# Kernel tuning notes

Measured on AMD Instinct MI355X. Metric: run time of the kernel, lower is better.

## Reference

```python
import jax, jax.numpy as jnp
import numpy as np

VOCAB, DIM, LAYERS = 32000, 1024, 4
B, L = 8, 512


def setup_inputs() -> dict:
    key = jax.random.key(0)
    ks = jax.random.split(key, 8)
    s = 0.02
    return {
        "input_ids": jax.random.randint(ks[0], (B, L), 0, VOCAB),
        "embed_W": jax.random.normal(ks[1], (VOCAB, DIM), jnp.float32) * s,
        "h_starter": jax.random.normal(ks[2], (LAYERS, DIM), jnp.float32) * s,
        "gate_W": jax.random.normal(ks[3], (LAYERS, 2 * DIM, 2 * DIM), jnp.float32) * s,
        "gate_b": jnp.zeros((LAYERS, 2 * DIM), jnp.float32),
        "cand_W": jax.random.normal(ks[4], (LAYERS, DIM, 2 * DIM), jnp.float32) * s,
        "cand_b": jnp.zeros((LAYERS, DIM), jnp.float32),
        "out_W": jax.random.normal(ks[5], (VOCAB, DIM), jnp.float32) * s,
    }


def _gru_forward(input_ids, embed_W, h_starter, gate_W, gate_b, cand_W, cand_b, out_W):
    Bsz = input_ids.shape[0]
    x = embed_W[input_ids]                      # [B, L, D]
    h0 = jnp.broadcast_to(h_starter[:, None, :], (LAYERS, Bsz, DIM))  # [Ly, B, D]

    def step(h, x_t):
        # h: [Ly, B, D], x_t: [B, D]
        new_h = []
        xin = x_t
        for i in range(LAYERS):
            hi = h[i]
            xh = jnp.concatenate([xin, hi], axis=-1)           # [B, 2D]
            g = xh @ gate_W[i].T + gate_b[i]                   # [B, 2D]
            z, r = jnp.split(g, 2, axis=-1)
            z = jax.nn.sigmoid(z)
            r = jax.nn.sigmoid(r)
            cin = jnp.concatenate([xin, r * hi], axis=-1)      # [B, 2D]
            cand = jnp.tanh(cin @ cand_W[i].T + cand_b[i])     # [B, D]
            hn = z * hi + (1.0 - z) * cand
            new_h.append(hn)
            xin = hn
        return jnp.stack(new_h), xin

    _, ys = jax.lax.scan(step, h0, jnp.swapaxes(x, 0, 1))      # ys: [L, B, D]
    ys = jnp.swapaxes(ys, 0, 1)                                # [B, L, D]
    logits = jnp.einsum('bld,vd->blv', ys, out_W)              # [B, L, V]
    return logits


def reference(input_ids, embed_W, h_starter, gate_W, gate_b, cand_W, cand_b, out_W):
    return _gru_forward(input_ids, embed_W, h_starter, gate_W, gate_b, cand_W, cand_b, out_W)
```

## Files before the change

kernel.cpp:

```cpp
#include <hip/hip_runtime.h>
#include <hip/hip_bf16.h>

#define VOCAB  32000
#define DIM    1024
#define NLAYER 4
#define NB     8
#define SEQ    512

#define NGROUP       4
#define GBLKS        64
#define SCAN_BLOCKS  (NGROUP * GBLKS)
#define SCAN_THREADS 512
#define ROWH         2056

typedef __attribute__((ext_vector_type(8))) short          bf16x8;
typedef __attribute__((ext_vector_type(4))) float          f32x4;
typedef __attribute__((ext_vector_type(2))) float          f32x2;
typedef __attribute__((ext_vector_type(8))) unsigned short u16x8;
typedef __attribute__((ext_vector_type(4))) unsigned short u16x4;
typedef __attribute__((ext_vector_type(8))) _Float16       h8f;
typedef __attribute__((ext_vector_type(4))) _Float16       h4f;

__device__ __forceinline__ u16x8 cvt8_bf16(const float* p) {
    float4 f0 = *(const float4*)p;
    float4 f1 = *(const float4*)(p + 4);
    union { __hip_bfloat16 h[8]; u16x8 v; } u;
    u.h[0] = __float2bfloat16(f0.x); u.h[1] = __float2bfloat16(f0.y);
    u.h[2] = __float2bfloat16(f0.z); u.h[3] = __float2bfloat16(f0.w);
    u.h[4] = __float2bfloat16(f1.x); u.h[5] = __float2bfloat16(f1.y);
    u.h[6] = __float2bfloat16(f1.z); u.h[7] = __float2bfloat16(f1.w);
    return u.v;
}

__device__ __forceinline__ h8f pack8(f32x4 a, f32x4 b) {
    h8f o;
    o[0] = (_Float16)a[0]; o[1] = (_Float16)a[1];
    o[2] = (_Float16)a[2]; o[3] = (_Float16)a[3];
    o[4] = (_Float16)b[0]; o[5] = (_Float16)b[1];
    o[6] = (_Float16)b[2]; o[7] = (_Float16)b[3];
    return o;
}

__device__ __forceinline__ void ld4v(f32x4& d, const float* p) {
    asm volatile("global_load_dwordx4 %0, %1, off sc0 sc1"
                 : "=&v"(d) : "v"(p));
}
__device__ __forceinline__ void st8v(void* p, f32x2 v) {
    asm volatile("global_store_dwordx2 %0, %1, off sc0 sc1"
                 :: "v"(p), "v"(v) : "memory");
}
__device__ __forceinline__ void st2v(void* p, unsigned v) {
    asm volatile("global_store_short %0, %1, off sc0 sc1"
                 :: "v"(p), "v"(v) : "memory");
}
__device__ __forceinline__ void vmwait0() {
    asm volatile("s_waitcnt vmcnt(0)" ::: "memory");
}

__global__ void bar_init_kernel(unsigned* __restrict__ bar) {
    bar[threadIdx.x]        = 0u;
    bar[threadIdx.x + 1024] = 0u;
    bar[threadIdx.x + 2048] = 0u;
    bar[threadIdx.x + 3072] = 0u;
}

__device__ __forceinline__ void slot_bar(unsigned* __restrict__ slots, int bkg,
                                         unsigned seq, bool& dead) {
    __syncthreads();
    const int tid = threadIdx.x;
    if (tid == 0)
        __hip_atomic_store(&slots[bkg * 8], seq, __ATOMIC_RELAXED,
                           __HIP_MEMORY_SCOPE_AGENT);
    if (tid < 64 && !dead) {
        unsigned guard = 0;
        for (;;) {
            unsigned v = __hip_atomic_load(&slots[tid * 8], __ATOMIC_RELAXED,
                                           __HIP_MEMORY_SCOPE_AGENT);
            if (__all((int)(v >= seq))) break;
            __builtin_amdgcn_s_sleep(1);
            if (++guard > (1u << 16)) { dead = true; break; }
        }
    }
    __syncthreads();
}

__global__ void __launch_bounds__(SCAN_THREADS)
__attribute__((amdgpu_waves_per_eu(2, 2)))
gru_scan(
    const int*   __restrict__ ids,
    const float* __restrict__ embW,
    const float* __restrict__ hstart,
    const float* __restrict__ gW,
    const float* __restrict__ gB,
    const float* __restrict__ cW,
    const float* __restrict__ cB,
    _Float16* __restrict__ hbuf16,
    _Float16* __restrict__ rbuf16,
    __hip_bfloat16* __restrict__ ysfb,
    unsigned* __restrict__ bar,
    const float* __restrict__ outW,
    __hip_bfloat16* __restrict__ outWb,
    int doConv)
{
    __shared__ _Float16 act[NB][ROWH];
    __shared__ float pz[4][4][64];
    __shared__ float pr[4][4][64];
    __shared__ float pc[2][4][64];
    __shared__ float pcb[2][4][64];
    __shared__ float hb[4][64];

    const int tid   = threadIdx.x;
    const int lane  = tid & 63;
    const int wv    = tid >> 6;
    const int l15   = lane & 15;
    const int lgq   = lane >> 4;
    const int bcol  = l15 & 7;
    const int g     = blockIdx.x >> 6;
    const int bkg   = blockIdx.x & (GBLKS-1);
    const int jbase = bkg * 16;
    const int jrow  = jbase + l15;

    if (doConv && g > 0) {
        const int cidx = (blockIdx.x - GBLKS) * SCAN_THREADS + tid;
        for (int u = cidx; u < VOCAB * DIM / 8; u += (SCAN_BLOCKS - GBLKS) * SCAN_THREADS)
            ((u16x8*)outWb)[u] = cvt8_bf16(outW + (size_t)u * 8);
    }

    h8f Wa[16], Wb[16];
    if (wv < 6) {
        const float* wzp = gW + ((size_t)g * 2048 + jrow) * 2048;
        const float* wrp = gW + ((size_t)g * 2048 + 1024 + jrow) * 2048;
        const float* wcp = cW + ((size_t)g * 1024 + jrow) * 2048;
        const float* baseA; const float* baseB; int koA, koB;
        switch (wv) {
          case 0:  baseA = wzp; koA = 0;    baseB = wrp; koB = 0;    break;
          case 1:  baseA = wzp; koA = 512;  baseB = wrp; koB = 512;  break;
          case 2:  baseA = wzp; koA = 1024; baseB = wrp; koB = 1024; break;
          case 3:  baseA = wzp; koA = 1536; baseB = wrp; koB = 1536; break;
          case 4:  baseA = wcp; koA = 0;    baseB = wcp; koB = 1024; break;
          default: baseA = wcp; koA = 512;  baseB = wcp; koB = 1536; break;
        }
        #pragma unroll
        for (int kc = 0; kc < 16; ++kc) {
            const int ka = koA + kc * 32 + lgq * 8;
            const int kb = koB + kc * 32 + lgq * 8;
            Wa[kc] = pack8(*(const f32x4*)(baseA + ka), *(const f32x4*)(baseA + ka + 4));
            Wb[kc] = pack8(*(const f32x4*)(baseB + kb), *(const f32x4*)(baseB + kb + 4));
        }
        #pragma unroll
        for (int kc = 0; kc < 16; ++kc) {
            asm volatile("" : "+v"(Wa[kc]));
            asm volatile("" : "+v"(Wb[kc]));
        }
    }

    float bz4[4], br4[4], cb4[4], hold[4], zreg[4];
    if (wv == 6) {
        #pragma unroll
        for (int r = 0; r < 4; ++r) {
            const int j = jbase + lgq * 4 + r;
            bz4[r]  = gB[g * 2048 + j];
            cb4[r]  = cB[g * 1024 + j];
            hold[r] = hstart[g * 1024 + j];
            hb[r][lane] = hold[r];
        }
    }
    if (wv == 7) {
        #pragma unroll
        for (int r = 0; r < 4; ++r)
            br4[r] = gB[g * 2048 + 1024 + jbase + lgq * 4 + r];
    }

    bool dead = false;
    unsigned* slots1g = bar + g * 512;
    unsigned* slots2g = bar + 2048 + g * 512;
    unsigned* s2prev  = (g > 0)          ? bar + 2048 + (g - 1) * 512 : nullptr;
    unsigned* s1next  = (g < NGROUP - 1) ? bar + (g + 1) * 512        : nullptr;
    _Float16* rbufg16 = rbuf16 + (size_t)g * NB * DIM;

    if (tid < 128) {
        int e = bkg * 128 + tid;
        union { _Float16 h; unsigned short u; } cv;
        cv.h = (_Float16)hstart[g * DIM + (e & (DIM - 1))];
        st2v(&hbuf16[((size_t)3 * NLAYER + g) * NB * DIM + e], (unsigned)cv.u);
    }
    slot_bar(slots2g, bkg, 1u, dead);

    for (int t = 0; t < SEQ; ++t) {
        const int so = (t + 3) & 3;
        const int sw = t & 3;
        const _Float16* hsrc16  = hbuf16 + ((size_t)so * NLAYER + g) * NB * DIM;
        _Float16*       hdst16  = hbuf16 + ((size_t)sw * NLAYER + g) * NB * DIM;
        const _Float16* xprev16 = hbuf16 + ((size_t)sw * NLAYER + (g > 0 ? g - 1 : 0)) * NB * DIM;

        {
            const unsigned need_a = (g > 0) ? (unsigned)(t + 2) : 0u;
            const unsigned need_b = (g < NGROUP - 1 && t >= 4) ? (unsigned)(t - 3) : 0u;
            if (tid < 64 && !dead && (need_a | need_b)) {
                unsigned guard = 0;
                for (;;) {
                    bool ok = true;
                    if (need_a)
                        ok &= (__hip_atomic_load(&s2prev[tid * 8], __ATOMIC_RELAXED,
                                                 __HIP_MEMORY_SCOPE_AGENT) >= need_a);
                    if (need_b)
                        ok &= (__hip_atomic_load(&s1next[tid * 8], __ATOMIC_RELAXED,
                                                 __HIP_MEMORY_SCOPE_AGENT) >= need_b);
                    if (__all((int)ok)) break;
                    __builtin_amdgcn_s_sleep(1);
                    if (++guard > (1u << 16)) { dead = true; break; }
                }
            }
            __syncthreads();
        }

        if (g == 0) {
            #pragma unroll
            for (int q = 0; q < 2; ++q) {
                const int u = q * SCAN_THREADS + tid;
                const int b = u >> 7, d8 = (u & 127) * 8;
                const float* p = embW + (size_t)ids[b * SEQ + t] * DIM + d8;
                *(h8f*)&act[b][d8] = pack8(*(const f32x4*)p, *(const f32x4*)(p + 4));
            }
            f32x4 hv[2];
            #pragma unroll
            for (int q = 0; q < 2; ++q) {
                const int u = q * SCAN_THREADS + tid;
                ld4v(hv[q], (const float*)(hsrc16 + (size_t)(u >> 7) * DIM + (u & 127) * 8));
            }
            vmwait0();
            asm volatile("" : "+v"(hv[0]), "+v"(hv[1]));
            #pragma unroll
            for (int q = 0; q < 2; ++q) {
                const int u = q * SCAN_THREADS + tid;
                *(h8f*)&act[u >> 7][1024 + (u & 127) * 8] = __builtin_bit_cast(h8f, hv[q]);
            }
        } else {
            f32x4 xv[2], hv[2];
            #pragma unroll
            for (int q = 0; q < 2; ++q) {
                const int u = q * SCAN_THREADS + tid;
                ld4v(xv[q], (const float*)(xprev16 + (size_t)(u >> 7) * DIM + (u & 127) * 8));
                ld4v(hv[q], (const float*)(hsrc16 + (size_t)(u >> 7) * DIM + (u & 127) * 8));
            }
            vmwait0();
            asm volatile("" : "+v"(xv[0]), "+v"(xv[1]), "+v"(hv[0]), "+v"(hv[1]));
            #pragma unroll
            for (int q = 0; q < 2; ++q) {
                const int u = q * SCAN_THREADS + tid;
                const int b = u >> 7, d8 = (u & 127) * 8;
                *(h8f*)&act[b][d8]        = __builtin_bit_cast(h8f, xv[q]);
                *(h8f*)&act[b][1024 + d8] = __builtin_bit_cast(h8f, hv[q]);
            }
        }
        __syncthreads();

        if (wv < 6) {
            const int kb2 = (wv < 4) ? wv * 512 : (wv - 4) * 512;
            f32x4 accA = {0.f, 0.f, 0.f, 0.f};
            f32x4 accB = {0.f, 0.f, 0.f, 0.f};
            #pragma unroll
            for (int kc = 0; kc < 16; ++kc) {
                const h8f bf = *(const h8f*)&act[bcol][kb2 + kc * 32 + lgq * 8];
                accA = __builtin_amdgcn_mfma_f32_16x16x32_f16(Wa[kc], bf, accA, 0, 0, 0);
                if (wv < 4)
                    accB = __builtin_amdgcn_mfma_f32_16x16x32_f16(Wb[kc], bf, accB, 0, 0, 0);
            }
            if (wv < 4) {
                #pragma unroll
                for (int r = 0; r < 4; ++r) {
                    pz[wv][r][lane] = accA[r];
                    pr[wv][r][lane] = accB[r];
                }
            } else {
                #pragma unroll
                for (int r = 0; r < 4; ++r) pc[wv - 4][r][lane] = accA[r];
            }
        }
        __syncthreads();

        if (wv == 6) {
            #pragma unroll
            for (int r = 0; r < 4; ++r) {
                const float s = pz[0][r][lane] + pz[1][r][lane]
                              + pz[2][r][lane] + pz[3][r][lane] + bz4[r];
                zreg[r] = 1.f / (1.f + expf(-s));
            }
        }
        if (wv == 7) {
            h4f rh4;
            #pragma unroll
            for (int r = 0; r < 4; ++r) {
                const float s = pr[0][r][lane] + pr[1][r][lane]
                              + pr[2][r][lane] + pr[3][r][lane] + br4[r];
                const float rg = 1.f / (1.f + expf(-s));
                rh4[r] = (_Float16)(rg * hb[r][lane]);
            }
            if (l15 < 8)
                st8v(rbufg16 + (size_t)bcol * DIM + jbase + lgq * 4,
                     __builtin_bit_cast(f32x2, rh4));
        }
        slot_bar(slots1g, bkg, (unsigned)(t + 1), dead);

        {
            f32x4 rv[2];
            #pragma unroll
            for (int q = 0; q < 2; ++q) {
                const int u = q * SCAN_THREADS + tid;
                ld4v(rv[q], (const float*)(rbufg16 + (size_t)(u >> 7) * DIM + (u & 127) * 8));
            }
            vmwait0();
            asm volatile("" : "+v"(rv[0]), "+v"(rv[1]));
            #pragma unroll
            for (int q = 0; q < 2; ++q) {
                const int u = q * SCAN_THREADS + tid;
                *(h8f*)&act[u >> 7][(u & 127) * 8] = __builtin_bit_cast(h8f, rv[q]);
            }
        }
        __syncthreads();

        if (wv == 4 || wv == 5) {
            const int kb2 = (wv - 4) * 512;
            f32x4 acc = {0.f, 0.f, 0.f, 0.f};
            #pragma unroll
            for (int kc = 0; kc < 16; ++kc) {
                const h8f bf = *(const h8f*)&act[bcol][kb2 + kc * 32 + lgq * 8];
                acc = __builtin_amdgcn_mfma_f32_16x16x32_f16(Wb[kc], bf, acc, 0, 0, 0);
            }
            #pragma unroll
            for (int r = 0; r < 4; ++r) pcb[wv - 4][r][lane] = acc[r];
        }
        __syncthreads();

        if (wv == 6) {
            h4f hp; u16x4 yp;
            #pragma unroll
            for (int r = 0; r < 4; ++r) {
                const float cand = tanhf(pc[0][r][lane] + pc[1][r][lane]
                                         + pcb[0][r][lane] + pcb[1][r][lane] + cb4[r]);
                const float hn = zreg[r] * hold[r] + (1.f - zreg[r]) * cand;
                hold[r] = hn;
                hb[r][lane] = hn;
                hp[r] = (_Float16)hn;
                union { __hip_bfloat16 b; unsigned short u; } cv;
                cv.b = __float2bfloat16(hn);
                yp[r] = cv.u;
            }
            if (l15 < 8) {
                st8v(hdst16 + (size_t)bcol * DIM + jbase + lgq * 4,
                     __builtin_bit_cast(f32x2, hp));
                if (g == NGROUP - 1)
                    *(f32x2*)(ysfb + ((size_t)bcol * SEQ + t) * DIM + jbase + lgq * 4) =
                        __builtin_bit_cast(f32x2, yp);
            }
        }
        slot_bar(slots2g, bkg, (unsigned)(t + 2), dead);
    }

    if (dead && tid == 0) {
        union { __hip_bfloat16 b; unsigned short u; } cv;
        cv.b = __float2bfloat16(1.0e8f);
        ((unsigned short*)ysfb)[blockIdx.x] = cv.u;
    }
}

#define BM 128
#define BN 128
#define BK 64

__global__ void __launch_bounds__(256) out_gemm_bb(
    const __hip_bfloat16* __restrict__ A,
    const __hip_bfloat16* __restrict__ B,
    float* __restrict__ C)
{
    __shared__ __hip_bfloat16 At[BM][BK + 8];
    __shared__ __hip_bfloat16 Bt[BN][BK + 8];

    const int tid  = threadIdx.x;
    const int lane = tid & 63;
    const int wv   = tid >> 6;
    const int wm   = wv >> 1, wn = wv & 1;
    const int m0   = blockIdx.y * BM;
    const int n0   = blockIdx.x * BN;

    f32x4 acc[4][4];
    #pragma unroll
    for (int i = 0; i < 4; ++i)
        #pragma unroll
        for (int jj = 0; jj < 4; ++jj)
            acc[i][jj] = (f32x4){0.f, 0.f, 0.f, 0.f};

    const int srow = tid >> 3;
    const int scol = (tid & 7) * 8;
    const int l15  = lane & 15;
    const int l4   = lane >> 4;

    for (int kt = 0; kt < DIM / BK; ++kt) {
        const int k0 = kt * BK;
        #pragma unroll
        for (int rnd = 0; rnd < 4; ++rnd) {
            const int row = rnd * 32 + srow;
            *(u16x8*)&At[row][scol] =
                *(const u16x8*)&A[(size_t)(m0 + row) * DIM + k0 + scol];
            *(u16x8*)&Bt[row][scol] =
                *(const u16x8*)&B[(size_t)(n0 + row) * DIM + k0 + scol];
        }
        __syncthreads();
        #pragma unroll
        for (int ks = 0; ks < 2; ++ks) {
            bf16x8 av[4], bv[4];
            #pragma unroll
            for (int i = 0; i < 4; ++i) {
                av[i] = *(const bf16x8*)&At[wm * 64 + i * 16 + l15][ks * 32 + l4 * 8];
                bv[i] = *(const bf16x8*)&Bt[wn * 64 + i * 16 + l15][ks * 32 + l4 * 8];
            }
            #pragma unroll
            for (int i = 0; i < 4; ++i)
                #pragma unroll
                for (int jj = 0; jj < 4; ++jj)
                    acc[i][jj] = __builtin_amdgcn_mfma_f32_16x16x32_bf16(
                        av[i], bv[jj], acc[i][jj], 0, 0, 0);
        }
        __syncthreads();
    }

    const int rq = l4 * 4;
    #pragma unroll
    for (int i = 0; i < 4; ++i) {
        const int rbase = m0 + wm * 64 + i * 16 + rq;
        #pragma unroll
        for (int jj = 0; jj < 4; ++jj) {
            const int col = n0 + wn * 64 + jj * 16 + l15;
            #pragma unroll
            for (int r2 = 0; r2 < 4; ++r2)
                C[(size_t)(rbase + r2) * VOCAB + col] = acc[i][jj][r2];
        }
    }
}

__global__ void __launch_bounds__(256) out_gemm_bf(
    const __hip_bfloat16* __restrict__ A,
    const float* __restrict__ B,
    float* __restrict__ C)
{
    __shared__ __hip_bfloat16 At[BM][BK + 8];
    __shared__ __hip_bfloat16 Bt[BN][BK + 8];

    const int tid  = threadIdx.x;
    const int lane = tid & 63;
    const int wv   = tid >> 6;
    const int wm   = wv >> 1, wn = wv & 1;
    const int m0   = blockIdx.y * BM;
    const int n0   = blockIdx.x * BN;

    f32x4 acc[4][4];
    #pragma unroll
    for (int i = 0; i < 4; ++i)
        #pragma unroll
        for (int jj = 0; jj < 4; ++jj)
            acc[i][jj] = (f32x4){0.f, 0.f, 0.f, 0.f};

    const int srow = tid >> 3;
    const int scol = (tid & 7) * 8;
    const int l15  = lane & 15;
    const int l4   = lane >> 4;

    for (int kt = 0; kt < DIM / BK; ++kt) {
        const int k0 = kt * BK;
        #pragma unroll
        for (int rnd = 0; rnd < 4; ++rnd) {
            const int row = rnd * 32 + srow;
            *(u16x8*)&At[row][scol] =
                *(const u16x8*)&A[(size_t)(m0 + row) * DIM + k0 + scol];
            *(u16x8*)&Bt[row][scol] =
                cvt8_bf16(&B[(size_t)(n0 + row) * DIM + k0 + scol]);
        }
        __syncthreads();
        #pragma unroll
        for (int ks = 0; ks < 2; ++ks) {
            bf16x8 av[4], bv[4];
            #pragma unroll
            for (int i = 0; i < 4; ++i) {
                av[i] = *(const bf16x8*)&At[wm * 64 + i * 16 + l15][ks * 32 + l4 * 8];
                bv[i] = *(const bf16x8*)&Bt[wn * 64 + i * 16 + l15][ks * 32 + l4 * 8];
            }
            #pragma unroll
            for (int i = 0; i < 4; ++i)
                #pragma unroll
                for (int jj = 0; jj < 4; ++jj)
                    acc[i][jj] = __builtin_amdgcn_mfma_f32_16x16x32_bf16(
                        av[i], bv[jj], acc[i][jj], 0, 0, 0);
        }
        __syncthreads();
    }

    const int rq = l4 * 4;
    #pragma unroll
    for (int i = 0; i < 4; ++i) {
        const int rbase = m0 + wm * 64 + i * 16 + rq;
        #pragma unroll
        for (int jj = 0; jj < 4; ++jj) {
            const int col = n0 + wn * 64 + jj * 16 + l15;
            #pragma unroll
            for (int r2 = 0; r2 < 4; ++r2)
                C[(size_t)(rbase + r2) * VOCAB + col] = acc[i][jj][r2];
        }
    }
}

extern "C" void kernel_launch(void* const* d_in, const int* in_sizes, int n_in,
                              void* d_out, int out_size, void* d_ws, size_t ws_size,
                              hipStream_t stream)
{
    (void)in_sizes; (void)n_in; (void)out_size;
    const int*   ids  = (const int*)  d_in[0];
    const float* embW = (const float*)d_in[1];
    const float* hst  = (const float*)d_in[2];
    const float* gW   = (const float*)d_in[3];
    const float* gB   = (const float*)d_in[4];
    const float* cW   = (const float*)d_in[5];
    const float* cB   = (const float*)d_in[6];
    const float* outW = (const float*)d_in[7];
    float* logits = (float*)d_out;

    char* ws = (char*)d_ws;
    unsigned*       bar    = (unsigned*)ws;
    _Float16*       rbuf16 = (_Float16*)(ws + 16384);
    _Float16*       hbuf16 = (_Float16*)(ws + 16384 + 65536);
    __hip_bfloat16* ysfb   = (__hip_bfloat16*)(ws + 16384 + 65536 + 262144);
    const size_t outWb_off = 16384 + 65536 + 262144 + (size_t)NB * SEQ * DIM * 2;
    const size_t need      = outWb_off + (size_t)VOCAB * DIM * 2;
    const int doConv = (ws_size >= need) ? 1 : 0;
    __hip_bfloat16* outWb = doConv ? (__hip_bfloat16*)(ws + outWb_off) : nullptr;

    bar_init_kernel<<<dim3(1), dim3(1024), 0, stream>>>(bar);

    gru_scan<<<dim3(SCAN_BLOCKS), dim3(SCAN_THREADS), 0, stream>>>(
        ids, embW, hst, gW, gB, cW, cB, hbuf16, rbuf16, ysfb, bar,
        outW, outWb, doConv);

    if (doConv)
        out_gemm_bb<<<dim3(VOCAB / BN, (NB * SEQ) / BM), dim3(256), 0, stream>>>(
            ysfb, outWb, logits);
    else
        out_gemm_bf<<<dim3(VOCAB / BN, (NB * SEQ) / BM), dim3(256), 0, stream>>>(
            ysfb, outW, logits);
}
```

Measured before the change: 3.504 ms.

## Use direct global-to-LDS loads and XCD-aware block swizzle in output GEMM

The output projection GEMM now stages A and B tiles with global_load_lds (buffer-to-LDS DMA) instead of going through registers, and drops the LDS row padding the direct load needs. The launch grid is flattened to 1D and remapped so consecutive blocks on the same XCD share tiles, which should improve L2 reuse. Without padding the MFMA fragment reads from LDS may hit bank conflicts. The GRU scan dominates runtime, so the effect on total time is bounded.

```diff
diff --git a/kernel.cpp b/kernel.cpp
--- a/kernel.cpp
+++ b/kernel.cpp
@@ -55,6 +55,12 @@
 }
 __device__ __forceinline__ void vmwait0() {
     asm volatile("s_waitcnt vmcnt(0)" ::: "memory");
+}
+
+__device__ __forceinline__ void gload_lds16(const void* g, void* l) {
+    __builtin_amdgcn_global_load_lds(
+        (const __attribute__((address_space(1))) void*)g,
+        (__attribute__((address_space(3))) void*)l, 16, 0, 0);
 }
 
 __global__ void bar_init_kernel(unsigned* __restrict__ bar) {
@@ -373,15 +379,19 @@
     const __hip_bfloat16* __restrict__ B,
     float* __restrict__ C)
 {
-    __shared__ __hip_bfloat16 At[BM][BK + 8];
-    __shared__ __hip_bfloat16 Bt[BN][BK + 8];
+    __shared__ __hip_bfloat16 At[BM][BK];
+    __shared__ __hip_bfloat16 Bt[BN][BK];
 
     const int tid  = threadIdx.x;
     const int lane = tid & 63;
     const int wv   = tid >> 6;
     const int wm   = wv >> 1, wn = wv & 1;
-    const int m0   = blockIdx.y * BM;
-    const int n0   = blockIdx.x * BN;
+    const int l15  = lane & 15;
+    const int l4   = lane >> 4;
+
+    const int swz = (blockIdx.x & 7) * 1000 + (blockIdx.x >> 3);
+    const int n0  = (swz % 250) * BN;
+    const int m0  = (swz / 250) * BM;
 
     f32x4 acc[4][4];
     #pragma unroll
@@ -390,20 +400,18 @@
         for (int jj = 0; jj < 4; ++jj)
             acc[i][jj] = (f32x4){0.f, 0.f, 0.f, 0.f};
 
-    const int srow = tid >> 3;
+    const int srow = (tid >> 3);
     const int scol = (tid & 7) * 8;
-    const int l15  = lane & 15;
-    const int l4   = lane >> 4;
 
     for (int kt = 0; kt < DIM / BK; ++kt) {
         const int k0 = kt * BK;
         #pragma unroll
-        for (int rnd = 0; rnd < 4; ++rnd) {
-            const int row = rnd * 32 + srow;
-            *(u16x8*)&At[row][scol] =
-                *(const u16x8*)&A[(size_t)(m0 + row) * DIM + k0 + scol];
-            *(u16x8*)&Bt[row][scol] =
-                *(const u16x8*)&B[(size_t)(n0 + row) * DIM + k0 + scol];
+        for (int r = 0; r < 4; ++r) {
+            const int row = r * 32 + srow;
+            gload_lds16(&A[(size_t)(m0 + row) * DIM + k0 + scol],
+                        &At[r * 32 + wv * 8][0]);
+            gload_lds16(&B[(size_t)(n0 + row) * DIM + k0 + scol],
+                        &Bt[r * 32 + wv * 8][0]);
         }
         __syncthreads();
         #pragma unroll
@@ -540,7 +548,7 @@
         outW, outWb, doConv);
 
     if (doConv)
-        out_gemm_bb<<<dim3(VOCAB / BN, (NB * SEQ) / BM), dim3(256), 0, stream>>>(
+        out_gemm_bb<<<dim3((VOCAB / BN) * ((NB * SEQ) / BM)), dim3(256), 0, stream>>>(
             ysfb, outWb, logits);
     else
         out_gemm_bf<<<dim3(VOCAB / BN, (NB * SEQ) / BM), dim3(256), 0, stream>>>(
```

Result: no change. 3.480 ms (-0.7%).
